# Optimization experiments

Hardware: AMD Instinct MI355X
Metric: run time of the kernel (lower is better)

## Reference

```python
import jax, jax.numpy as jnp
import numpy as np

E, N, D, H = 600000, 100000, 128, 128
LN_EPS = 1e-5


def setup_inputs() -> dict:
    key = jax.random.key(0)
    ks = jax.random.split(key, 10)
    inp = {
        "efeat": jax.random.normal(ks[0], (E, D), dtype=jnp.float32),
        "nfeat": jax.random.normal(ks[1], (N, D), dtype=jnp.float32),
        "src_idx": jax.random.randint(ks[2], (E,), 0, N, dtype=jnp.int64) if jax.config.jax_enable_x64 else jax.random.randint(ks[2], (E,), 0, N, dtype=jnp.int32),
        "dst_idx": jax.random.randint(ks[3], (E,), 0, N, dtype=jnp.int32),
        # MLP params: Linear(3D -> H) + SiLU, Linear(H -> D), LayerNorm(D)
        "W1": jax.random.normal(ks[4], (3 * D, H), dtype=jnp.float32) / np.sqrt(3 * D),
        "b1": jnp.zeros((H,), dtype=jnp.float32),
        "W2": jax.random.normal(ks[5], (H, D), dtype=jnp.float32) / np.sqrt(H),
        "b2": jnp.zeros((D,), dtype=jnp.float32),
        "ln_scale": jnp.ones((D,), dtype=jnp.float32),
        "ln_bias": jnp.zeros((D,), dtype=jnp.float32),
    }
    return inp


def _layernorm(x, scale, bias):
    mu = jnp.mean(x, axis=-1, keepdims=True)
    var = jnp.mean(jnp.square(x - mu), axis=-1, keepdims=True)
    return (x - mu) * jax.lax.rsqrt(var + LN_EPS) * scale + bias


def reference(efeat, nfeat, src_idx, dst_idx, W1, b1, W2, b2, ln_scale, ln_bias):
    # Gather per-edge source/destination node features (irregular access).
    src = nfeat[src_idx]              # [E, D]
    dst = nfeat[dst_idx]              # [E, D]
    # TMLP: equivalent to concat([efeat, src, dst]) @ W1; expressed as split GEMMs
    # so no [E, 3D] concat buffer is materialized.
    Wf, Ws, Wd = W1[:D], W1[D:2 * D], W1[2 * D:]
    h = efeat @ Wf + src @ Ws + dst @ Wd + b1   # [E, H]
    h = jax.nn.silu(h)
    y = h @ W2 + b2                              # [E, D]
    y = _layernorm(y, ln_scale, ln_bias)
    efeat_new = y + efeat                        # residual add
    return (efeat_new, nfeat)
```

## Files before the change

kernel.cpp:

```cpp
#include <hip/hip_runtime.h>
#include <stdint.h>

#define E_N 600000
#define N_N 100000

typedef short short8   __attribute__((ext_vector_type(8)));
typedef short short8a  __attribute__((ext_vector_type(8), may_alias));
typedef float floatx4  __attribute__((ext_vector_type(4)));
typedef float floatx2  __attribute__((ext_vector_type(2)));
typedef float floatx4a __attribute__((ext_vector_type(4), may_alias));
typedef float floatx8a __attribute__((ext_vector_type(8), may_alias));
typedef unsigned int uintx2  __attribute__((ext_vector_type(2)));
typedef unsigned int uintx2a __attribute__((ext_vector_type(2), may_alias));
typedef unsigned int uintx4a __attribute__((ext_vector_type(4), may_alias));
typedef __bf16 bf16x4 __attribute__((ext_vector_type(4)));
typedef __bf16 bf16x8 __attribute__((ext_vector_type(8)));

static __device__ __forceinline__ unsigned short f2bf(float f){
  unsigned u = __builtin_bit_cast(unsigned, f);
  unsigned rnd = 0x7fffu + ((u >> 16) & 1u);
  return (unsigned short)((u + rnd) >> 16);
}
static __device__ __forceinline__ unsigned pk2(float a, float b){
  floatx2 f; f[0] = a; f[1] = b;
  typedef __bf16 bf16x2 __attribute__((ext_vector_type(2)));
  return __builtin_bit_cast(unsigned, __builtin_convertvector(f, bf16x2));
}

__global__ void prep_weights(const float* __restrict__ W1, const float* __restrict__ W2,
                             unsigned short* __restrict__ w1s, unsigned short* __restrict__ w2s){
  int i = blockIdx.x * 256 + threadIdx.x;
  if (i < 384 * 128){
    int c = i / 384, k = i - c * 384;
    int dw = c * 192 + ((k >> 1) ^ ((c & 7) << 2));
    w1s[dw * 2 + (k & 1)] = f2bf(W1[k * 128 + c]);
  } else {
    int j = i - 384 * 128;
    int c = j >> 7, k = j & 127;
    int dw = c * 64 + ((k >> 1) ^ ((c & 7) << 2));
    w2s[dw * 2 + (k & 1)] = f2bf(W2[k * 128 + c]);
  }
}

__global__ void prep_nfeat(const float* __restrict__ nf,
                           unsigned* __restrict__ nfbu,
                           float* __restrict__ out2){
  const int total = N_N * 128 / 4;
  int stride = gridDim.x * blockDim.x;
  for (int i = blockIdx.x * blockDim.x + threadIdx.x; i < total; i += stride){
    float4 v = reinterpret_cast<const float4*>(nf)[i];
    reinterpret_cast<float4*>(out2)[i] = v;
    nfbu[2 * i]     = pk2(v.x, v.y);
    nfbu[2 * i + 1] = pk2(v.z, v.w);
  }
}

static __device__ __forceinline__ void glds16(void* lds, const void* g){
  __builtin_amdgcn_global_load_lds((const __attribute__((address_space(1))) unsigned int*)g,
                                   (__attribute__((address_space(3))) unsigned int*)lds,
                                   16, 0, 0);
}

__global__ __launch_bounds__(512, 2) void fused_edge(
    const float* __restrict__ efeat,
    const int* __restrict__ src_idx, const int* __restrict__ dst_idx,
    const unsigned short* __restrict__ nfb,
    const unsigned short* __restrict__ w1s, const unsigned short* __restrict__ w2s,
    const float* __restrict__ b1, const float* __restrict__ b2,
    const float* __restrict__ lns, const float* __restrict__ lnb,
    float* __restrict__ out)
{
  __shared__ __align__(16) unsigned char smem[133120];
  unsigned int* wlds  = (unsigned int*)smem;
  float*        cmisc = (float*)(smem + 131072);

  const int tid  = threadIdx.x;
  const int w    = tid >> 6;
  const int lane = tid & 63;
  const int r    = lane & 15;
  const int g    = lane >> 4;
  const int sw8  = (r & 7) << 2;

  unsigned int* tile = (unsigned int*)(smem + 98304 + w * 4096);

  #pragma unroll
  for (int rnd = 0; rnd < 12; ++rnd){
    int off = rnd * 8192 + tid * 16;
    glds16(smem + off, (const unsigned char*)w1s + off);
  }
  cmisc[tid] = tid < 128 ? b1[tid] : tid < 256 ? b2[tid - 128]
             : tid < 384 ? lns[tid - 256] : lnb[tid - 384];

  const int eb = blockIdx.x * 512 + w * 64;

  int er[4];
  #pragma unroll
  for (int e2 = 0; e2 < 4; ++e2){
    int e = eb + 16 * e2 + r;
    er[e2] = e < E_N ? e : (E_N - 1);
  }
  int gidx[2][4];
  #pragma unroll
  for (int e2 = 0; e2 < 4; ++e2){
    int si = src_idx[er[e2]];
    int di = dst_idx[er[e2]];
    si = si < 0 ? 0 : (si >= N_N ? N_N - 1 : si);
    di = di < 0 ? 0 : (di >= N_N ? N_N - 1 : di);
    gidx[0][e2] = si;
    gidx[1][e2] = di;
  }

  __syncthreads();

  auto loadX_f32 = [&](const float* p) -> short8 {
    floatx8a f = *reinterpret_cast<const floatx8a*>(p);
    return __builtin_bit_cast(short8, __builtin_convertvector(f, bf16x8));
  };
  auto loadW1L = [&](int mi, int kf) -> short8 {
    uintx4a v = *reinterpret_cast<const uintx4a*>(
        &wlds[(16 * mi + r) * 192 + ((kf * 16 + 4 * g) ^ sw8)]);
    return __builtin_bit_cast(short8, v);
  };
  auto loadW2L = [&](int mo, int ks) -> short8 {
    uintx4a v = *reinterpret_cast<const uintx4a*>(
        &wlds[(16 * mo + r) * 64 + ((ks * 16 + 4 * g) ^ sw8)]);
    return __builtin_bit_cast(short8, v);
  };

  floatx4 acc1[4][8];
  #pragma unroll
  for (int e2 = 0; e2 < 4; ++e2)
    #pragma unroll
    for (int mi = 0; mi < 8; ++mi)
      acc1[e2][mi] = (floatx4){0.f, 0.f, 0.f, 0.f};

  #pragma unroll
  for (int kf = 0; kf < 12; ++kf){
    short8 x[4];
    #pragma unroll
    for (int e2 = 0; e2 < 4; ++e2){
      if (kf < 4)
        x[e2] = loadX_f32(efeat + (size_t)er[e2] * 128 + kf * 32 + 8 * g);
      else if (kf < 8)
        x[e2] = *reinterpret_cast<const short8a*>(nfb + (size_t)gidx[0][e2] * 128 + (kf - 4) * 32 + 8 * g);
      else
        x[e2] = *reinterpret_cast<const short8a*>(nfb + (size_t)gidx[1][e2] * 128 + (kf - 8) * 32 + 8 * g);
    }
    #pragma unroll
    for (int mi = 0; mi < 8; ++mi){
      short8 wf = loadW1L(mi, kf);
      #pragma unroll
      for (int e2 = 0; e2 < 4; ++e2)
        acc1[e2][mi] = __builtin_amdgcn_mfma_f32_16x16x32_bf16(wf, x[e2], acc1[e2][mi], 0, 0, 0);
    }
  }

  __syncthreads();
  #pragma unroll
  for (int rnd = 0; rnd < 4; ++rnd){
    int off = rnd * 8192 + tid * 16;
    glds16(smem + off, (const unsigned char*)w2s + off);
  }

  auto epi1 = [&](int e2){
    #pragma unroll
    for (int mi = 0; mi < 8; ++mi){
      floatx4 bb = *reinterpret_cast<const floatx4a*>(&cmisc[16 * mi + 4 * g]);
      floatx4 vv;
      #pragma unroll
      for (int q = 0; q < 4; ++q){
        float xx = acc1[e2][mi][q] + bb[q];
        vv[q] = xx * __builtin_amdgcn_rcpf(1.f + __expf(-xx));
      }
      uintx2 pk = __builtin_bit_cast(uintx2, __builtin_convertvector(vv, bf16x4));
      *reinterpret_cast<uintx2a*>(&tile[r * 64 + ((8 * mi + 2 * g) ^ sw8)]) = pk;
    }
  };
  epi1(0);

  __syncthreads();

  #pragma unroll
  for (int e2 = 0; e2 < 4; ++e2){
    if (e2 > 0) epi1(e2);

    floatx4 acc2[8];
    #pragma unroll
    for (int mo = 0; mo < 8; ++mo)
      acc2[mo] = (floatx4){0.f, 0.f, 0.f, 0.f};

    #pragma unroll
    for (int ks = 0; ks < 4; ++ks){
      uintx4a hv = *reinterpret_cast<const uintx4a*>(&tile[r * 64 + ((ks * 16 + 4 * g) ^ sw8)]);
      short8 hb = __builtin_bit_cast(short8, hv);
      #pragma unroll
      for (int mo = 0; mo < 8; ++mo){
        short8 wf = loadW2L(mo, ks);
        acc2[mo] = __builtin_amdgcn_mfma_f32_16x16x32_bf16(wf, hb, acc2[mo], 0, 0, 0);
      }
    }

    float s1 = 0.f, s2 = 0.f;
    #pragma unroll
    for (int mo = 0; mo < 8; ++mo){
      floatx4 bb = *reinterpret_cast<const floatx4a*>(&cmisc[128 + 16 * mo + 4 * g]);
      #pragma unroll
      for (int q = 0; q < 4; ++q){
        float v = acc2[mo][q] + bb[q];
        s1 += v; s2 += v * v;
      }
    }
    s1 += __shfl_xor(s1, 16); s2 += __shfl_xor(s2, 16);
    s1 += __shfl_xor(s1, 32); s2 += __shfl_xor(s2, 32);

    float mu   = s1 * (1.f / 128.f);
    float var  = s2 * (1.f / 128.f) - mu * mu;
    var = var > 0.f ? var : 0.f;
    float rstd = __builtin_amdgcn_rsqf(var + 1e-5f);

    int e = eb + 16 * e2 + r;
    if (e < E_N){
      const float* ef = efeat + (size_t)e * 128;
      float*       op = out   + (size_t)e * 128;
      #pragma unroll
      for (int mo = 0; mo < 8; ++mo){
        int c = 16 * mo + 4 * g;
        floatx4 bb = *reinterpret_cast<const floatx4a*>(&cmisc[128 + c]);
        floatx4 ls = *reinterpret_cast<const floatx4a*>(&cmisc[256 + c]);
        floatx4 lb = *reinterpret_cast<const floatx4a*>(&cmisc[384 + c]);
        floatx4 e4 = *reinterpret_cast<const floatx4a*>(ef + c);
        floatx4 o4;
        #pragma unroll
        for (int q = 0; q < 4; ++q)
          o4[q] = (acc2[mo][q] + bb[q] - mu) * rstd * ls[q] + lb[q] + e4[q];
        *reinterpret_cast<floatx4a*>(op + c) = o4;
      }
    }
  }
}

extern "C" void kernel_launch(void* const* d_in, const int* in_sizes, int n_in,
                              void* d_out, int out_size, void* d_ws, size_t ws_size,
                              hipStream_t stream){
  const float* efeat = (const float*)d_in[0];
  const float* nfeat = (const float*)d_in[1];
  const int*   srci  = (const int*)d_in[2];
  const int*   dsti  = (const int*)d_in[3];
  const float* W1    = (const float*)d_in[4];
  const float* b1    = (const float*)d_in[5];
  const float* W2    = (const float*)d_in[6];
  const float* b2    = (const float*)d_in[7];
  const float* lns   = (const float*)d_in[8];
  const float* lnb   = (const float*)d_in[9];
  float* out = (float*)d_out;

  char* ws = (char*)d_ws;
  unsigned short* w1s = (unsigned short*)ws;
  unsigned short* w2s = (unsigned short*)(ws + 98304);
  unsigned short* nfb = (unsigned short*)(ws + 131072);

  prep_weights<<<(384 * 128 + 128 * 128) / 256, 256, 0, stream>>>(W1, W2, w1s, w2s);
  prep_nfeat<<<2048, 256, 0, stream>>>(nfeat, (unsigned*)nfb, out + (size_t)E_N * 128);

  int blocks = (E_N + 511) / 512;
  fused_edge<<<blocks, 512, 0, stream>>>(efeat, srci, dsti, nfb, w1s, w2s,
                                         b1, b2, lns, lnb, out);
}
```

Baseline: 259.4 us.

## Stream W1 through LDS in K-chunks and halve edges per block

```diff
diff --git a/kernel.cpp b/kernel.cpp
--- a/kernel.cpp
+++ b/kernel.cpp
@@ -32,8 +32,9 @@
   int i = blockIdx.x * 256 + threadIdx.x;
   if (i < 384 * 128){
     int c = i / 384, k = i - c * 384;
-    int dw = c * 192 + ((k >> 1) ^ ((c & 7) << 2));
-    w1s[dw * 2 + (k & 1)] = f2bf(W1[k * 128 + c]);
+    int p = k >> 7, kp = k & 127;
+    int dw = c * 64 + ((kp >> 1) ^ ((c & 7) << 2));
+    w1s[p * 16384 + dw * 2 + (k & 1)] = f2bf(W1[k * 128 + c]);
   } else {
     int j = i - 384 * 128;
     int c = j >> 7, k = j & 127;
@@ -61,7 +62,7 @@
                                    16, 0, 0);
 }
 
-__global__ __launch_bounds__(512, 2) void fused_edge(
+__global__ __launch_bounds__(512, 4) void fused_edge(
     const float* __restrict__ efeat,
     const int* __restrict__ src_idx, const int* __restrict__ dst_idx,
     const unsigned short* __restrict__ nfb,
@@ -70,9 +71,9 @@
     const float* __restrict__ lns, const float* __restrict__ lnb,
     float* __restrict__ out)
 {
-  __shared__ __align__(16) unsigned char smem[133120];
+  __shared__ __align__(16) unsigned char smem[67584];
   unsigned int* wlds  = (unsigned int*)smem;
-  float*        cmisc = (float*)(smem + 131072);
+  float*        cmisc = (float*)(smem + 65536);
 
   const int tid  = threadIdx.x;
   const int w    = tid >> 6;
@@ -81,27 +82,31 @@
   const int g    = lane >> 4;
   const int sw8  = (r & 7) << 2;
 
-  unsigned int* tile = (unsigned int*)(smem + 98304 + w * 4096);
-
-  #pragma unroll
-  for (int rnd = 0; rnd < 12; ++rnd){
-    int off = rnd * 8192 + tid * 16;
-    glds16(smem + off, (const unsigned char*)w1s + off);
-  }
+  unsigned int* tile = (unsigned int*)(smem + 32768 + w * 4096);
+
+  auto stageW = [&](const unsigned short* src){
+    #pragma unroll
+    for (int rnd = 0; rnd < 4; ++rnd){
+      int off = rnd * 8192 + tid * 16;
+      glds16(smem + off, (const unsigned char*)src + off);
+    }
+  };
+
+  stageW(w1s);
   cmisc[tid] = tid < 128 ? b1[tid] : tid < 256 ? b2[tid - 128]
              : tid < 384 ? lns[tid - 256] : lnb[tid - 384];
 
-  const int eb = blockIdx.x * 512 + w * 64;
-
-  int er[4];
-  #pragma unroll
-  for (int e2 = 0; e2 < 4; ++e2){
+  const int eb = blockIdx.x * 256 + w * 32;
+
+  int er[2];
+  #pragma unroll
+  for (int e2 = 0; e2 < 2; ++e2){
     int e = eb + 16 * e2 + r;
     er[e2] = e < E_N ? e : (E_N - 1);
   }
-  int gidx[2][4];
-  #pragma unroll
-  for (int e2 = 0; e2 < 4; ++e2){
+  int gidx[2][2];
+  #pragma unroll
+  for (int e2 = 0; e2 < 2; ++e2){
     int si = src_idx[er[e2]];
     int di = dst_idx[er[e2]];
     si = si < 0 ? 0 : (si >= N_N ? N_N - 1 : si);
@@ -116,51 +121,18 @@
     floatx8a f = *reinterpret_cast<const floatx8a*>(p);
     return __builtin_bit_cast(short8, __builtin_convertvector(f, bf16x8));
   };
-  auto loadW1L = [&](int mi, int kf) -> short8 {
+  auto loadWL = [&](int m, int k4) -> short8 {
     uintx4a v = *reinterpret_cast<const uintx4a*>(
-        &wlds[(16 * mi + r) * 192 + ((kf * 16 + 4 * g) ^ sw8)]);
+        &wlds[(16 * m + r) * 64 + ((k4 * 16 + 4 * g) ^ sw8)]);
     return __builtin_bit_cast(short8, v);
   };
-  auto loadW2L = [&](int mo, int ks) -> short8 {
-    uintx4a v = *reinterpret_cast<const uintx4a*>(
-        &wlds[(16 * mo + r) * 64 + ((ks * 16 + 4 * g) ^ sw8)]);
-    return __builtin_bit_cast(short8, v);
-  };
-
-  floatx4 acc1[4][8];
-  #pragma unroll
-  for (int e2 = 0; e2 < 4; ++e2)
+
+  floatx4 acc1[2][8];
+  #pragma unroll
+  for (int e2 = 0; e2 < 2; ++e2)
     #pragma unroll
     for (int mi = 0; mi < 8; ++mi)
       acc1[e2][mi] = (floatx4){0.f, 0.f, 0.f, 0.f};
-
-  #pragma unroll
-  for (int kf = 0; kf < 12; ++kf){
-    short8 x[4];
-    #pragma unroll
-    for (int e2 = 0; e2 < 4; ++e2){
-      if (kf < 4)
-        x[e2] = loadX_f32(efeat + (size_t)er[e2] * 128 + kf * 32 + 8 * g);
-      else if (kf < 8)
-        x[e2] = *reinterpret_cast<const short8a*>(nfb + (size_t)gidx[0][e2] * 128 + (kf - 4) * 32 + 8 * g);
-      else
-        x[e2] = *reinterpret_cast<const short8a*>(nfb + (size_t)gidx[1][e2] * 128 + (kf - 8) * 32 + 8 * g);
-    }
-    #pragma unroll
-    for (int mi = 0; mi < 8; ++mi){
-      short8 wf = loadW1L(mi, kf);
-      #pragma unroll
-      for (int e2 = 0; e2 < 4; ++e2)
-        acc1[e2][mi] = __builtin_amdgcn_mfma_f32_16x16x32_bf16(wf, x[e2], acc1[e2][mi], 0, 0, 0);
-    }
-  }
-
-  __syncthreads();
-  #pragma unroll
-  for (int rnd = 0; rnd < 4; ++rnd){
-    int off = rnd * 8192 + tid * 16;
-    glds16(smem + off, (const unsigned char*)w2s + off);
-  }
 
   auto epi1 = [&](int e2){
     #pragma unroll
@@ -176,12 +148,38 @@
       *reinterpret_cast<uintx2a*>(&tile[r * 64 + ((8 * mi + 2 * g) ^ sw8)]) = pk;
     }
   };
-  epi1(0);
-
-  __syncthreads();
-
-  #pragma unroll
-  for (int e2 = 0; e2 < 4; ++e2){
+
+  #pragma unroll
+  for (int p = 0; p < 3; ++p){
+    #pragma unroll
+    for (int k4 = 0; k4 < 4; ++k4){
+      const int kf = p * 4 + k4;
+      short8 x[2];
+      #pragma unroll
+      for (int e2 = 0; e2 < 2; ++e2){
+        if (kf < 4)
+          x[e2] = loadX_f32(efeat + (size_t)er[e2] * 128 + kf * 32 + 8 * g);
+        else if (kf < 8)
+          x[e2] = *reinterpret_cast<const short8a*>(nfb + (size_t)gidx[0][e2] * 128 + (kf - 4) * 32 + 8 * g);
+        else
+          x[e2] = *reinterpret_cast<const short8a*>(nfb + (size_t)gidx[1][e2] * 128 + (kf - 8) * 32 + 8 * g);
+      }
+      #pragma unroll
+      for (int mi = 0; mi < 8; ++mi){
+        short8 wf = loadWL(mi, k4);
+        acc1[0][mi] = __builtin_amdgcn_mfma_f32_16x16x32_bf16(wf, x[0], acc1[0][mi], 0, 0, 0);
+        acc1[1][mi] = __builtin_amdgcn_mfma_f32_16x16x32_bf16(wf, x[1], acc1[1][mi], 0, 0, 0);
+      }
+    }
+    __syncthreads();
+    if (p < 2) stageW(w1s + (p + 1) * 16384);
+    else       stageW(w2s);
+    if (p == 2) epi1(0);
+    __syncthreads();
+  }
+
+  #pragma unroll
+  for (int e2 = 0; e2 < 2; ++e2){
     if (e2 > 0) epi1(e2);
 
     floatx4 acc2[8];
@@ -195,7 +193,7 @@
       short8 hb = __builtin_bit_cast(short8, hv);
       #pragma unroll
       for (int mo = 0; mo < 8; ++mo){
-        short8 wf = loadW2L(mo, ks);
+        short8 wf = loadWL(mo, ks);
         acc2[mo] = __builtin_amdgcn_mfma_f32_16x16x32_bf16(wf, hb, acc2[mo], 0, 0, 0);
       }
     }
@@ -262,7 +260,7 @@
   prep_weights<<<(384 * 128 + 128 * 128) / 256, 256, 0, stream>>>(W1, W2, w1s, w2s);
   prep_nfeat<<<2048, 256, 0, stream>>>(nfeat, (unsigned*)nfb, out + (size_t)E_N * 128);
 
-  int blocks = (E_N + 511) / 512;
+  int blocks = (E_N + 255) / 256;
   fused_edge<<<blocks, 512, 0, stream>>>(efeat, srci, dsti, nfb, w1s, w2s,
                                          b1, b2, lns, lnb, out);
 }
```

Result: slower. 336.2 us (+29.6%).
